# Performance work log

Hardware: AMD Instinct MI355X
Metric: run time of the kernel (lower is better)

The kernel has to match this reference:

```python
import jax, jax.numpy as jnp
import numpy as np

B, T, H, NSPK = 8, 1024, 1024, 2
LN_EPS = 1e-5


def setup_inputs() -> dict:
    key = jax.random.key(0)
    ks = jax.random.split(key, 12)
    s = 1.0 / np.sqrt(H)
    return {
        "x": jax.random.normal(ks[0], (B, T, H), jnp.float32),
        "qmask": jax.random.uniform(ks[1], (B, T, NSPK), jnp.float32),
        "dia_len": jax.random.randint(ks[2], (B,), T // 2, T + 1),
        "wp": 8,
        "wf": 8,
        "W_msg": jax.random.normal(ks[3], (H, H), jnp.float32) * s,
        "b_msg": jax.random.normal(ks[4], (H,), jnp.float32) * s,
        "W_self": jax.random.normal(ks[5], (H, H), jnp.float32) * s,
        "b_self": jax.random.normal(ks[6], (H,), jnp.float32) * s,
        "W_out": jax.random.normal(ks[7], (H, H), jnp.float32) * s,
        "b_out": jax.random.normal(ks[8], (H,), jnp.float32) * s,
        "gamma": jnp.ones((H,), jnp.float32),
        "beta": jnp.zeros((H,), jnp.float32),
    }


def reference(x, qmask, dia_len, wp, wf, W_msg, b_msg, W_self, b_self, W_out, b_out, gamma, beta):
    Bb, Tt, Hh = x.shape
    spk = jnp.argmax(qmask, axis=-1)                     # [B,T]
    pos = jnp.arange(Tt)
    offs = jnp.arange(-wp, wf + 1)                       # [W]
    idx = pos[:, None] + offs[None, :]                   # [T,W] window indices
    vlen = dia_len[:, None, None]                        # [B,1,1]
    valid = (idx[None] >= 0) & (idx[None] <= vlen - 1)   # [B,T,W]
    idxc = jnp.clip(idx, 0, Tt - 1)
    nb = jnp.take(x, idxc, axis=1)                       # [B,T,W,H]
    nb_spk = jnp.take(spk, idxc, axis=1)                 # [B,T,W]
    same = (nb_spk == spk[:, :, None]).astype(x.dtype)
    w = jnp.where(valid, 0.5 + 0.5 * same, 0.0)          # speaker weights, masked
    cnt = jnp.maximum(valid.sum(-1).astype(x.dtype), 1.0)  # window sizes [B,T]
    msg = jnp.einsum('btw,btwh->bth', w, nb) / cnt[..., None]
    h = x @ W_self + b_self + msg @ W_msg + b_msg        # per-node fusion
    node_valid = (pos[None, :] < dia_len[:, None])[..., None]
    out = jnp.where(node_valid, h, x)                    # nodes past dia_len keep x
    y = jax.nn.relu(out) @ W_out + b_out                 # dropout = identity (eval)
    z = x + y
    mean = z.mean(-1, keepdims=True)
    var = z.var(-1, keepdims=True)
    return gamma * (z - mean) / jnp.sqrt(var + LN_EPS) + beta
```

## Files before the change

kernel.cpp:

```cpp
#include <hip/hip_runtime.h>


typedef unsigned short u16;
typedef float floatx4 __attribute__((ext_vector_type(4)));
typedef short shortx8 __attribute__((ext_vector_type(8)));

#define T_ 1024
#define H_ 1024

__device__ __forceinline__ float bf2f(u16 v) {
    return __uint_as_float(((unsigned)v) << 16);
}
__device__ __forceinline__ u16 f2bf(float f) {
    unsigned u = __float_as_uint(f);
    return (u16)((u + 0x7fffu + ((u >> 16) & 1u)) >> 16);
}
__device__ __forceinline__ void async16(const void* g, void* l) {
    __builtin_amdgcn_global_load_lds(
        (__attribute__((address_space(1))) void*)g,
        (__attribute__((address_space(3))) void*)l, 16, 0, 0);
}

__global__ __launch_bounds__(256)
void transpose_pack(const float* __restrict__ Wself, const float* __restrict__ Wmsg,
                    const float* __restrict__ Wout,
                    u16* __restrict__ wt_cat, u16* __restrict__ wt_out)
{
    __shared__ float s[32][33];
    const int wid = blockIdx.z;
    const float* src = (wid == 0) ? Wself : ((wid == 1) ? Wmsg : Wout);
    const int n0 = blockIdx.x * 32, k0 = blockIdx.y * 32;
    const int tx = threadIdx.x & 31, ty = threadIdx.x >> 5;
#pragma unroll
    for (int i = 0; i < 4; ++i) {
        int k = k0 + ty + 8 * i;
        s[ty + 8 * i][tx] = src[(size_t)k * H_ + n0 + tx];
    }
    __syncthreads();
#pragma unroll
    for (int i = 0; i < 4; ++i) {
        int n = n0 + ty + 8 * i;
        u16 v = f2bf(s[tx][ty + 8 * i]);
        if (wid < 2) wt_cat[(size_t)n * 2048 + wid * 1024 + k0 + tx] = v;
        else         wt_out[(size_t)n * 1024 + k0 + tx] = v;
    }
}

__global__ __launch_bounds__(256)
void msg_pack(const float* __restrict__ x, const float* __restrict__ qmask,
              const int* __restrict__ dia_len, u16* __restrict__ xcat)
{
    __shared__ u16 sx[32][1024];
    const int tid = threadIdx.x;
    const int b = blockIdx.y;
    const int t0 = blockIdx.x * 16;
    const int dlen = dia_len[b];
    const int c4 = tid * 4;
    const float* xb = x + (size_t)b * T_ * H_;

    unsigned spkmask = 0;
#pragma unroll 4
    for (int r = 0; r < 32; ++r) {
        int row = t0 - 8 + r;
        row = row < 0 ? 0 : (row > T_ - 1 ? T_ - 1 : row);
        const float* q = qmask + ((size_t)b * T_ + row) * 2;
        spkmask |= (q[1] > q[0] ? 1u : 0u) << r;
        float4 v = *(const float4*)(xb + (size_t)row * H_ + c4);
        ushort4 u;
        u.x = f2bf(v.x); u.y = f2bf(v.y); u.z = f2bf(v.z); u.w = f2bf(v.w);
        *(ushort4*)&sx[r][c4] = u;
    }
    __syncthreads();

    for (int lt = 0; lt < 16; ++lt) {
        const int t = t0 + lt;
        const unsigned cs = (spkmask >> (lt + 8)) & 1u;
        float a0 = 0.f, a1 = 0.f, a2 = 0.f, a3 = 0.f;
        int cnt = 0;
#pragma unroll
        for (int o = 0; o < 17; ++o) {
            const int idx = t + o - 8;
            if (idx >= 0 && idx < dlen) {
                const float w = (((spkmask >> (lt + o)) & 1u) == cs) ? 1.0f : 0.5f;
                ++cnt;
                ushort4 u = *(const ushort4*)&sx[lt + o][c4];
                a0 += w * bf2f(u.x); a1 += w * bf2f(u.y);
                a2 += w * bf2f(u.z); a3 += w * bf2f(u.w);
            }
        }
        const float inv = 1.0f / (float)(cnt > 0 ? cnt : 1);
        ushort4 m;
        m.x = f2bf(a0 * inv); m.y = f2bf(a1 * inv);
        m.z = f2bf(a2 * inv); m.w = f2bf(a3 * inv);
        const size_t rowg = (size_t)b * T_ + t;
        *(ushort4*)&xcat[rowg * 2048 + 1024 + c4] = m;
        *(ushort4*)&xcat[rowg * 2048 + c4] = *(const ushort4*)&sx[lt + 8][c4];
    }
}

template <int K, int EPI>
__global__ __launch_bounds__(256)
void gemm_bt(const u16* __restrict__ A, const u16* __restrict__ Bt,
             const float* __restrict__ bias1, const float* __restrict__ bias2,
             const float* __restrict__ X, const int* __restrict__ dia_len,
             u16* __restrict__ Rout, float* __restrict__ Zout)
{
    __shared__ u16 sA[128 * 32];
    __shared__ u16 sB[128 * 32];
    const int tid = threadIdx.x;
    const int bn = blockIdx.x * 128;
    const int bm = blockIdx.y * 128;
    const int wave = tid >> 6, lane = tid & 63;
    const int wr = wave >> 1, wc = wave & 1;
    const int lrow = lane & 15, lq = lane >> 4;

    const u16* gA0 = A + (size_t)(bm + (tid >> 2)) * K + (tid & 3) * 8;
    const u16* gA1 = gA0 + (size_t)64 * K;
    const u16* gB0 = Bt + (size_t)(bn + (tid >> 2)) * K + (tid & 3) * 8;
    const u16* gB1 = gB0 + (size_t)64 * K;
    u16* lA = sA + wave * 512;
    u16* lB = sB + wave * 512;

    floatx4 acc[4][4];
#pragma unroll
    for (int i = 0; i < 4; ++i)
#pragma unroll
        for (int j = 0; j < 4; ++j)
            acc[i][j] = (floatx4){0.f, 0.f, 0.f, 0.f};

    const u16* pa = sA + (wr * 64 + lrow) * 32 + lq * 8;
    const u16* pb = sB + (wc * 64 + lrow) * 32 + lq * 8;

    for (int k0 = 0; k0 < K; k0 += 32) {
        __syncthreads();
        async16(gA0 + k0, lA);
        async16(gA1 + k0, lA + 2048);
        async16(gB0 + k0, lB);
        async16(gB1 + k0, lB + 2048);
        __syncthreads();
        shortx8 av[4], bv[4];
#pragma unroll
        for (int i = 0; i < 4; ++i) av[i] = *(const shortx8*)(pa + i * 512);
#pragma unroll
        for (int j = 0; j < 4; ++j) bv[j] = *(const shortx8*)(pb + j * 512);
#pragma unroll
        for (int i = 0; i < 4; ++i)
#pragma unroll
            for (int j = 0; j < 4; ++j)
                acc[i][j] = __builtin_amdgcn_mfma_f32_16x16x32_bf16(
                    av[i], bv[j], acc[i][j], 0, 0, 0);
    }

    const int dl = (EPI == 1) ? dia_len[bm >> 10] : 0;
#pragma unroll
    for (int i = 0; i < 4; ++i) {
        const int row0 = bm + wr * 64 + i * 16 + lq * 4;
#pragma unroll
        for (int j = 0; j < 4; ++j) {
            const int col = bn + wc * 64 + j * 16 + lrow;
#pragma unroll
            for (int r = 0; r < 4; ++r) {
                const int row = row0 + r;
                const float v = acc[i][j][r];
                if (EPI == 1) {
                    const float h = v + bias1[col] + bias2[col];
                    const float xv = X[(size_t)row * H_ + col];
                    const float outv = ((row & (T_ - 1)) < dl) ? h : xv;
                    Rout[(size_t)row * H_ + col] = f2bf(fmaxf(outv, 0.f));
                } else {
                    const float z = X[(size_t)row * H_ + col] + v + bias1[col];
                    Zout[(size_t)row * H_ + col] = z;
                }
            }
        }
    }
}

__global__ __launch_bounds__(256)
void ln_kernel(const float* __restrict__ Z, const float* __restrict__ gamma,
               const float* __restrict__ beta, float* __restrict__ out)
{
    const int row = blockIdx.x;
    const int tid = threadIdx.x;
    const size_t base = (size_t)row * H_ + tid * 4;
    float4 v = *(const float4*)(Z + base);
    float s = v.x + v.y + v.z + v.w;
    float q = v.x * v.x + v.y * v.y + v.z * v.z + v.w * v.w;
#pragma unroll
    for (int off = 32; off > 0; off >>= 1) {
        s += __shfl_down(s, off);
        q += __shfl_down(q, off);
    }
    __shared__ float ps[4], pq[4];
    const int wave = tid >> 6, lane = tid & 63;
    if (lane == 0) { ps[wave] = s; pq[wave] = q; }
    __syncthreads();
    const float S = ps[0] + ps[1] + ps[2] + ps[3];
    const float Q = pq[0] + pq[1] + pq[2] + pq[3];
    const float mean = S * (1.0f / 1024.0f);
    const float var = Q * (1.0f / 1024.0f) - mean * mean;
    const float inv = rsqrtf(var + 1e-5f);
    float4 g = *(const float4*)(gamma + tid * 4);
    float4 bt = *(const float4*)(beta + tid * 4);
    float4 o;
    o.x = g.x * (v.x - mean) * inv + bt.x;
    o.y = g.y * (v.y - mean) * inv + bt.y;
    o.z = g.z * (v.z - mean) * inv + bt.z;
    o.w = g.w * (v.w - mean) * inv + bt.w;
    *(float4*)(out + base) = o;
}

extern "C" void kernel_launch(void* const* d_in, const int* in_sizes, int n_in,
                              void* d_out, int out_size, void* d_ws, size_t ws_size,
                              hipStream_t stream)
{
    (void)in_sizes; (void)n_in; (void)out_size; (void)ws_size;
    const float* x       = (const float*)d_in[0];
    const float* qmask   = (const float*)d_in[1];
    const int*   dia_len = (const int*)d_in[2];
    const float* W_msg   = (const float*)d_in[5];
    const float* b_msg   = (const float*)d_in[6];
    const float* W_self  = (const float*)d_in[7];
    const float* b_self  = (const float*)d_in[8];
    const float* W_out   = (const float*)d_in[9];
    const float* b_out   = (const float*)d_in[10];
    const float* gamma   = (const float*)d_in[11];
    const float* beta    = (const float*)d_in[12];
    float* out = (float*)d_out;

    char* ws = (char*)d_ws;
    u16*   xcat   = (u16*)ws;
    u16*   rbuf   = (u16*)(ws + (size_t)(32u << 20));
    u16*   wt_cat = (u16*)(ws + (size_t)(48u << 20));
    u16*   wt_out = (u16*)(ws + (size_t)(52u << 20));
    float* zbuf   = (float*)ws;

    transpose_pack<<<dim3(32, 32, 3), 256, 0, stream>>>(W_self, W_msg, W_out, wt_cat, wt_out);
    msg_pack<<<dim3(64, 8), 256, 0, stream>>>(x, qmask, dia_len, xcat);
    gemm_bt<2048, 1><<<dim3(8, 64), 256, 0, stream>>>(xcat, wt_cat, b_self, b_msg,
                                                      x, dia_len, rbuf, nullptr);
    gemm_bt<1024, 2><<<dim3(8, 64), 256, 0, stream>>>(rbuf, wt_out, b_out, nullptr,
                                                      x, nullptr, nullptr, zbuf);
    ln_kernel<<<dim3(8192), 256, 0, stream>>>(zbuf, gamma, beta, out);
}
```

Before: 228.9 us.

## Reorder message aggregation after projection and split-K the output GEMM

Exploits linearity to project x by concatenated W_self and W_msg first, then apply the speaker-weighted window aggregation on the projected message features in a combine kernel with biases, masking and ReLU. The output GEMM is split along K into two partial bf16 results that the layernorm kernel sums along with x and the bias. This simplifies GEMM epilogues and doubles grid size for the second GEMM, at the cost of an extra pack pass, an extra kernel, and additional bf16 rounding of intermediate products.

```diff
diff --git a/kernel.cpp b/kernel.cpp
--- a/kernel.cpp
+++ b/kernel.cpp
@@ -22,9 +22,19 @@
 }
 
 __global__ __launch_bounds__(256)
+void pack_x(const float* __restrict__ x, u16* __restrict__ xbf)
+{
+    const size_t i = ((size_t)blockIdx.x * 256 + threadIdx.x) * 4;
+    float4 v = *(const float4*)(x + i);
+    ushort4 o;
+    o.x = f2bf(v.x); o.y = f2bf(v.y); o.z = f2bf(v.z); o.w = f2bf(v.w);
+    *(ushort4*)(xbf + i) = o;
+}
+
+__global__ __launch_bounds__(256)
 void transpose_pack(const float* __restrict__ Wself, const float* __restrict__ Wmsg,
                     const float* __restrict__ Wout,
-                    u16* __restrict__ wt_cat, u16* __restrict__ wt_out)
+                    u16* __restrict__ wt1, u16* __restrict__ wt_out)
 {
     __shared__ float s[32][33];
     const int wid = blockIdx.z;
@@ -41,83 +51,31 @@
     for (int i = 0; i < 4; ++i) {
         int n = n0 + ty + 8 * i;
         u16 v = f2bf(s[tx][ty + 8 * i]);
-        if (wid < 2) wt_cat[(size_t)n * 2048 + wid * 1024 + k0 + tx] = v;
-        else         wt_out[(size_t)n * 1024 + k0 + tx] = v;
-    }
-}
-
-__global__ __launch_bounds__(256)
-void msg_pack(const float* __restrict__ x, const float* __restrict__ qmask,
-              const int* __restrict__ dia_len, u16* __restrict__ xcat)
-{
-    __shared__ u16 sx[32][1024];
-    const int tid = threadIdx.x;
-    const int b = blockIdx.y;
-    const int t0 = blockIdx.x * 16;
-    const int dlen = dia_len[b];
-    const int c4 = tid * 4;
-    const float* xb = x + (size_t)b * T_ * H_;
-
-    unsigned spkmask = 0;
-#pragma unroll 4
-    for (int r = 0; r < 32; ++r) {
-        int row = t0 - 8 + r;
-        row = row < 0 ? 0 : (row > T_ - 1 ? T_ - 1 : row);
-        const float* q = qmask + ((size_t)b * T_ + row) * 2;
-        spkmask |= (q[1] > q[0] ? 1u : 0u) << r;
-        float4 v = *(const float4*)(xb + (size_t)row * H_ + c4);
-        ushort4 u;
-        u.x = f2bf(v.x); u.y = f2bf(v.y); u.z = f2bf(v.z); u.w = f2bf(v.w);
-        *(ushort4*)&sx[r][c4] = u;
-    }
-    __syncthreads();
-
-    for (int lt = 0; lt < 16; ++lt) {
-        const int t = t0 + lt;
-        const unsigned cs = (spkmask >> (lt + 8)) & 1u;
-        float a0 = 0.f, a1 = 0.f, a2 = 0.f, a3 = 0.f;
-        int cnt = 0;
-#pragma unroll
-        for (int o = 0; o < 17; ++o) {
-            const int idx = t + o - 8;
-            if (idx >= 0 && idx < dlen) {
-                const float w = (((spkmask >> (lt + o)) & 1u) == cs) ? 1.0f : 0.5f;
-                ++cnt;
-                ushort4 u = *(const ushort4*)&sx[lt + o][c4];
-                a0 += w * bf2f(u.x); a1 += w * bf2f(u.y);
-                a2 += w * bf2f(u.z); a3 += w * bf2f(u.w);
-            }
-        }
-        const float inv = 1.0f / (float)(cnt > 0 ? cnt : 1);
-        ushort4 m;
-        m.x = f2bf(a0 * inv); m.y = f2bf(a1 * inv);
-        m.z = f2bf(a2 * inv); m.w = f2bf(a3 * inv);
-        const size_t rowg = (size_t)b * T_ + t;
-        *(ushort4*)&xcat[rowg * 2048 + 1024 + c4] = m;
-        *(ushort4*)&xcat[rowg * 2048 + c4] = *(const ushort4*)&sx[lt + 8][c4];
-    }
-}
-
-template <int K, int EPI>
+        if (wid == 0)      wt1[(size_t)n * 1024 + k0 + tx] = v;
+        else if (wid == 1) wt1[(size_t)(n + 1024) * 1024 + k0 + tx] = v;
+        else               wt_out[(size_t)n * 1024 + k0 + tx] = v;
+    }
+}
+
+template <int KLEN, int EPI>
 __global__ __launch_bounds__(256)
 void gemm_bt(const u16* __restrict__ A, const u16* __restrict__ Bt,
-             const float* __restrict__ bias1, const float* __restrict__ bias2,
-             const float* __restrict__ X, const int* __restrict__ dia_len,
-             u16* __restrict__ Rout, float* __restrict__ Zout)
+             u16* __restrict__ O0, u16* __restrict__ O1)
 {
     __shared__ u16 sA[128 * 32];
     __shared__ u16 sB[128 * 32];
     const int tid = threadIdx.x;
     const int bn = blockIdx.x * 128;
     const int bm = blockIdx.y * 128;
+    const int kb = blockIdx.z * KLEN;
     const int wave = tid >> 6, lane = tid & 63;
     const int wr = wave >> 1, wc = wave & 1;
     const int lrow = lane & 15, lq = lane >> 4;
 
-    const u16* gA0 = A + (size_t)(bm + (tid >> 2)) * K + (tid & 3) * 8;
-    const u16* gA1 = gA0 + (size_t)64 * K;
-    const u16* gB0 = Bt + (size_t)(bn + (tid >> 2)) * K + (tid & 3) * 8;
-    const u16* gB1 = gB0 + (size_t)64 * K;
+    const u16* gA0 = A + (size_t)(bm + (tid >> 2)) * 1024 + kb + (tid & 3) * 8;
+    const u16* gA1 = gA0 + (size_t)64 * 1024;
+    const u16* gB0 = Bt + (size_t)(bn + (tid >> 2)) * 1024 + kb + (tid & 3) * 8;
+    const u16* gB1 = gB0 + (size_t)64 * 1024;
     u16* lA = sA + wave * 512;
     u16* lB = sB + wave * 512;
 
@@ -131,7 +89,7 @@
     const u16* pa = sA + (wr * 64 + lrow) * 32 + lq * 8;
     const u16* pb = sB + (wc * 64 + lrow) * 32 + lq * 8;
 
-    for (int k0 = 0; k0 < K; k0 += 32) {
+    for (int k0 = 0; k0 < KLEN; k0 += 32) {
         __syncthreads();
         async16(gA0 + k0, lA);
         async16(gA1 + k0, lA + 2048);
@@ -151,39 +109,108 @@
                     av[i], bv[j], acc[i][j], 0, 0, 0);
     }
 
-    const int dl = (EPI == 1) ? dia_len[bm >> 10] : 0;
+    u16* O;
+    int cbase;
+    if (EPI == 0) { O = (bn < 1024) ? O0 : O1; cbase = bn & 1023; }
+    else          { O = blockIdx.z ? O1 : O0;  cbase = bn; }
 #pragma unroll
     for (int i = 0; i < 4; ++i) {
         const int row0 = bm + wr * 64 + i * 16 + lq * 4;
 #pragma unroll
         for (int j = 0; j < 4; ++j) {
-            const int col = bn + wc * 64 + j * 16 + lrow;
-#pragma unroll
-            for (int r = 0; r < 4; ++r) {
-                const int row = row0 + r;
-                const float v = acc[i][j][r];
-                if (EPI == 1) {
-                    const float h = v + bias1[col] + bias2[col];
-                    const float xv = X[(size_t)row * H_ + col];
-                    const float outv = ((row & (T_ - 1)) < dl) ? h : xv;
-                    Rout[(size_t)row * H_ + col] = f2bf(fmaxf(outv, 0.f));
-                } else {
-                    const float z = X[(size_t)row * H_ + col] + v + bias1[col];
-                    Zout[(size_t)row * H_ + col] = z;
-                }
+            const int col = cbase + wc * 64 + j * 16 + lrow;
+#pragma unroll
+            for (int r = 0; r < 4; ++r)
+                O[(size_t)(row0 + r) * 1024 + col] = f2bf(acc[i][j][r]);
+        }
+    }
+}
+
+__global__ __launch_bounds__(256)
+void combine(const u16* __restrict__ u, const u16* __restrict__ v,
+             const float* __restrict__ x, const float* __restrict__ qmask,
+             const int* __restrict__ dia_len, const float* __restrict__ b_self,
+             const float* __restrict__ b_msg, u16* __restrict__ r)
+{
+    __shared__ u16 sv[32][1024];
+    const int tid = threadIdx.x;
+    const int b = blockIdx.y;
+    const int t0 = blockIdx.x * 16;
+    const int dlen = dia_len[b];
+    const int c4 = tid * 4;
+
+    unsigned spkmask = 0;
+#pragma unroll 4
+    for (int rr = 0; rr < 32; ++rr) {
+        int row = t0 - 8 + rr;
+        row = row < 0 ? 0 : (row > T_ - 1 ? T_ - 1 : row);
+        const float* q = qmask + ((size_t)b * T_ + row) * 2;
+        spkmask |= (q[1] > q[0] ? 1u : 0u) << rr;
+        *(ushort4*)&sv[rr][c4] =
+            *(const ushort4*)(v + ((size_t)b * T_ + row) * 1024 + c4);
+    }
+    __syncthreads();
+
+    float4 bs;
+    {
+        float4 b1 = *(const float4*)(b_self + c4);
+        float4 b2 = *(const float4*)(b_msg + c4);
+        bs.x = b1.x + b2.x; bs.y = b1.y + b2.y;
+        bs.z = b1.z + b2.z; bs.w = b1.w + b2.w;
+    }
+
+    for (int lt = 0; lt < 16; ++lt) {
+        const int t = t0 + lt;
+        const unsigned cs = (spkmask >> (lt + 8)) & 1u;
+        float a0 = 0.f, a1 = 0.f, a2 = 0.f, a3 = 0.f;
+        int cnt = 0;
+#pragma unroll
+        for (int o = 0; o < 17; ++o) {
+            const int idx = t + o - 8;
+            if (idx >= 0 && idx < dlen) {
+                const float w = (((spkmask >> (lt + o)) & 1u) == cs) ? 1.0f : 0.5f;
+                ++cnt;
+                ushort4 uu = *(const ushort4*)&sv[lt + o][c4];
+                a0 += w * bf2f(uu.x); a1 += w * bf2f(uu.y);
+                a2 += w * bf2f(uu.z); a3 += w * bf2f(uu.w);
             }
         }
-    }
-}
-
-__global__ __launch_bounds__(256)
-void ln_kernel(const float* __restrict__ Z, const float* __restrict__ gamma,
-               const float* __restrict__ beta, float* __restrict__ out)
+        const float inv = 1.0f / (float)(cnt > 0 ? cnt : 1);
+        const size_t rowg = (size_t)b * T_ + t;
+        ushort4 u4 = *(const ushort4*)(u + rowg * 1024 + c4);
+        float4 xv = *(const float4*)(x + rowg * H_ + c4);
+        const bool sel = (t < dlen);
+        float h0 = bf2f(u4.x) + bs.x + a0 * inv;
+        float h1 = bf2f(u4.y) + bs.y + a1 * inv;
+        float h2 = bf2f(u4.z) + bs.z + a2 * inv;
+        float h3 = bf2f(u4.w) + bs.w + a3 * inv;
+        ushort4 out;
+        out.x = f2bf(fmaxf(sel ? h0 : xv.x, 0.f));
+        out.y = f2bf(fmaxf(sel ? h1 : xv.y, 0.f));
+        out.z = f2bf(fmaxf(sel ? h2 : xv.z, 0.f));
+        out.w = f2bf(fmaxf(sel ? h3 : xv.w, 0.f));
+        *(ushort4*)(r + rowg * 1024 + c4) = out;
+    }
+}
+
+__global__ __launch_bounds__(256)
+void ln_final(const u16* __restrict__ P0, const u16* __restrict__ P1,
+              const float* __restrict__ x, const float* __restrict__ b_out,
+              const float* __restrict__ gamma, const float* __restrict__ beta,
+              float* __restrict__ out)
 {
     const int row = blockIdx.x;
     const int tid = threadIdx.x;
     const size_t base = (size_t)row * H_ + tid * 4;
-    float4 v = *(const float4*)(Z + base);
+    float4 xv = *(const float4*)(x + base);
+    ushort4 p0 = *(const ushort4*)(P0 + base);
+    ushort4 p1 = *(const ushort4*)(P1 + base);
+    float4 bo = *(const float4*)(b_out + tid * 4);
+    float4 v;
+    v.x = xv.x + bf2f(p0.x) + bf2f(p1.x) + bo.x;
+    v.y = xv.y + bf2f(p0.y) + bf2f(p1.y) + bo.y;
+    v.z = xv.z + bf2f(p0.z) + bf2f(p1.z) + bo.z;
+    v.w = xv.w + bf2f(p0.w) + bf2f(p1.w) + bo.w;
     float s = v.x + v.y + v.z + v.w;
     float q = v.x * v.x + v.y * v.y + v.z * v.z + v.w * v.w;
 #pragma unroll
@@ -229,17 +256,21 @@
     float* out = (float*)d_out;
 
     char* ws = (char*)d_ws;
-    u16*   xcat   = (u16*)ws;
-    u16*   rbuf   = (u16*)(ws + (size_t)(32u << 20));
-    u16*   wt_cat = (u16*)(ws + (size_t)(48u << 20));
-    u16*   wt_out = (u16*)(ws + (size_t)(52u << 20));
-    float* zbuf   = (float*)ws;
-
-    transpose_pack<<<dim3(32, 32, 3), 256, 0, stream>>>(W_self, W_msg, W_out, wt_cat, wt_out);
-    msg_pack<<<dim3(64, 8), 256, 0, stream>>>(x, qmask, dia_len, xcat);
-    gemm_bt<2048, 1><<<dim3(8, 64), 256, 0, stream>>>(xcat, wt_cat, b_self, b_msg,
-                                                      x, dia_len, rbuf, nullptr);
-    gemm_bt<1024, 2><<<dim3(8, 64), 256, 0, stream>>>(rbuf, wt_out, b_out, nullptr,
-                                                      x, nullptr, nullptr, zbuf);
-    ln_kernel<<<dim3(8192), 256, 0, stream>>>(zbuf, gamma, beta, out);
-}
+    u16* region0 = (u16*)ws;
+    u16* region1 = (u16*)(ws + (size_t)(16u << 20));
+    u16* region2 = (u16*)(ws + (size_t)(32u << 20));
+    u16* wt1     = (u16*)(ws + (size_t)(48u << 20));
+    u16* wt_out  = (u16*)(ws + (size_t)(52u << 20));
+
+    pack_x<<<dim3(8192), 256, 0, stream>>>(x, region0);
+    transpose_pack<<<dim3(32, 32, 3), 256, 0, stream>>>(W_self, W_msg, W_out,
+                                                        wt1, wt_out);
+    gemm_bt<1024, 0><<<dim3(16, 64, 1), 256, 0, stream>>>(region0, wt1,
+                                                          region1, region2);
+    combine<<<dim3(64, 8), 256, 0, stream>>>(region1, region2, x, qmask,
+                                             dia_len, b_self, b_msg, region0);
+    gemm_bt<512, 1><<<dim3(8, 64, 2), 256, 0, stream>>>(region0, wt_out,
+                                                        region1, region2);
+    ln_final<<<dim3(8192), 256, 0, stream>>>(region1, region2, x, b_out,
+                                             gamma, beta, out);
+}
```

After: 238.9 us. +4.4%, slower.
